# Performance work log

Hardware: AMD Instinct MI355X
Metric: run time of the kernel (lower is better)

Reference implementation:

```python
import jax, jax.numpy as jnp
import numpy as np

B, S, D, H, E, K = 4, 2048, 1024, 4096, 8, 2


def setup_inputs() -> dict:
    key = jax.random.key(0)
    ks = jax.random.split(key, 8)
    scale = 0.02
    x = jax.random.normal(ks[0], (B, S, D), dtype=jnp.float32)
    gate_w = jax.random.normal(ks[1], (D, E), dtype=jnp.float32) * scale
    gate_b = jnp.zeros((E,), dtype=jnp.float32)
    w1 = jax.random.normal(ks[2], (E, D, H), dtype=jnp.float32) * scale
    b1 = jnp.zeros((E, H), dtype=jnp.float32)
    w2 = jax.random.normal(ks[3], (E, H, D), dtype=jnp.float32) * scale
    b2 = jnp.zeros((E, D), dtype=jnp.float32)
    return {"x": x, "gate_w": gate_w, "gate_b": gate_b,
            "w1": w1, "b1": b1, "w2": w2, "b2": b2}


def reference(x, gate_w, gate_b, w1, b1, w2, b2):
    b, s, d = x.shape
    xf = x.reshape(-1, d)                              # [T, D]
    T = xf.shape[0]
    gates = xf @ gate_w + gate_b                       # [T, E]
    scores, idx = jax.lax.top_k(gates, K)              # [T, K] each
    g = jax.nn.softmax(scores, axis=-1)                # softmax over top-k slots
    # Per-token, per-expert combine weight (top-k indices are distinct)
    Wte = jnp.zeros((T, E), dtype=xf.dtype).at[jnp.arange(T)[:, None], idx].add(g)
    # Loop over the small fixed expert set via scan, accumulating weighted outputs.
    def body(acc, p):
        w1e, b1e, w2e, b2e, we = p                     # we: [T]
        h = jax.nn.gelu(xf @ w1e + b1e, approximate=False)  # [T, H]
        y = h @ w2e + b2e                              # [T, D]
        return acc + we[:, None] * y, None
    out, _ = jax.lax.scan(body, jnp.zeros_like(xf), (w1, b1, w2, b2, Wte.T))
    return out.reshape(b, s, d)
```

## Files before the change

kernel.cpp:

```cpp
#include <hip/hip_runtime.h>
#include <hip/hip_bf16.h>

#define Bb 4
#define Ss 2048
#define Dd 1024
#define Hh 4096
#define Ee 8
#define Tt (Bb*Ss)

typedef __attribute__((ext_vector_type(8))) short short8;
typedef __attribute__((ext_vector_type(4))) float floatx4;
typedef unsigned short u16;
typedef unsigned int u32;

__device__ __forceinline__ u16 f2bf(float f) {
  union { float f; u32 u; } v; v.f = f;
  return (u16)((v.u + 0x7FFFu + ((v.u >> 16) & 1u)) >> 16);
}

__global__ __launch_bounds__(256) void cvt_x(const float* __restrict__ x, u16* __restrict__ xb) {
  size_t i = ((size_t)blockIdx.x * 256 + threadIdx.x) * 8;
  float4 a = *(const float4*)(x + i);
  float4 b = *(const float4*)(x + i + 4);
  union { u16 us[8]; uint4 v; } o;
  o.us[0] = f2bf(a.x); o.us[1] = f2bf(a.y); o.us[2] = f2bf(a.z); o.us[3] = f2bf(a.w);
  o.us[4] = f2bf(b.x); o.us[5] = f2bf(b.y); o.us[6] = f2bf(b.z); o.us[7] = f2bf(b.w);
  *(uint4*)(xb + i) = o.v;
}

__global__ __launch_bounds__(256) void tconv(const float* __restrict__ src, u16* __restrict__ dst,
                                             int R, int C) {
  __shared__ float tile[64][65];
  int e = blockIdx.z;
  int r0 = blockIdx.y * 64, c0 = blockIdx.x * 64;
  int tx = threadIdx.x & 63, ty = threadIdx.x >> 6;
  const float* s = src + (size_t)e * R * C;
  u16* d = dst + (size_t)e * R * C;
#pragma unroll
  for (int i = 0; i < 16; i++) {
    int r = i * 4 + ty;
    tile[r][tx] = s[(size_t)(r0 + r) * C + c0 + tx];
  }
  __syncthreads();
#pragma unroll
  for (int i = 0; i < 16; i++) {
    int c = i * 4 + ty;
    d[(size_t)(c0 + c) * R + r0 + tx] = f2bf(tile[tx][c]);
  }
}

__global__ __launch_bounds__(256) void gate_kernel(const float* __restrict__ x,
                                                   const float* __restrict__ gw,
                                                   const float* __restrict__ gb,
                                                   int* __restrict__ counts,
                                                   int* __restrict__ tokL,
                                                   int* __restrict__ pairL,
                                                   float* __restrict__ wtL) {
  __shared__ float gwl[Dd * Ee];
  for (int i = threadIdx.x; i < Dd * Ee; i += 256) gwl[i] = gw[i];
  __syncthreads();
  int wid = threadIdx.x >> 6, lane = threadIdx.x & 63;
  int t = blockIdx.x * 4 + wid;
  const float* xr = x + (size_t)t * Dd;
  double acc[Ee];
#pragma unroll
  for (int e = 0; e < Ee; e++) acc[e] = 0.0;
  for (int i = 0; i < Dd / 64; i++) {
    int d = lane + i * 64;
    float xv = xr[d];
#pragma unroll
    for (int e = 0; e < Ee; e++) acc[e] += (double)xv * (double)gwl[d * Ee + e];
  }
#pragma unroll
  for (int off = 32; off > 0; off >>= 1)
#pragma unroll
    for (int e = 0; e < Ee; e++) acc[e] += __shfl_down(acc[e], off);
  if (lane == 0) {
    float s[Ee];
#pragma unroll
    for (int e = 0; e < Ee; e++) s[e] = (float)acc[e] + gb[e];
    int i0 = 0;
#pragma unroll
    for (int e = 1; e < Ee; e++) if (s[e] > s[i0]) i0 = e;
    int i1 = (i0 == 0) ? 1 : 0;
#pragma unroll
    for (int e = 0; e < Ee; e++) if (e != i0 && s[e] > s[i1]) i1 = e;
    float ex = expf(s[i1] - s[i0]);
    float g0 = 1.0f / (1.0f + ex);
    float g1 = ex / (1.0f + ex);
    int p0 = atomicAdd(&counts[i0], 1);
    tokL[i0 * Tt + p0] = t; pairL[i0 * Tt + p0] = t * 2;     wtL[i0 * Tt + p0] = g0;
    int p1 = atomicAdd(&counts[i1], 1);
    tokL[i1 * Tt + p1] = t; pairL[i1 * Tt + p1] = t * 2 + 1; wtL[i1 * Tt + p1] = g1;
  }
}

__global__ __launch_bounds__(256) void gemm1(const u16* __restrict__ xb,
                                             const u16* __restrict__ w1t,
                                             const float* __restrict__ b1,
                                             const int* __restrict__ counts,
                                             const int* __restrict__ tokL,
                                             const int* __restrict__ pairL,
                                             u16* __restrict__ h) {
  int e = blockIdx.z;
  int cnt = counts[e];
  int m0 = blockIdx.y * 128;
  if (m0 >= cnt) return;
  int rows = cnt - m0; if (rows > 128) rows = 128;
  int n0 = blockIdx.x * 128;

  __shared__ __align__(16) u16 As[128 * 40];
  __shared__ __align__(16) u16 Bs[128 * 40];
  __shared__ int ltok[128];
  __shared__ int lpair[128];

  int tid = threadIdx.x;
  if (tid < 128) {
    int ok = tid < rows;
    ltok[tid]  = ok ? tokL[e * Tt + m0 + tid] : 0;
    lpair[tid] = ok ? pairL[e * Tt + m0 + tid] : 0;
  }
  __syncthreads();

  floatx4 zero4 = {0.f, 0.f, 0.f, 0.f};
  floatx4 acc[4][4];
#pragma unroll
  for (int i = 0; i < 4; i++)
#pragma unroll
    for (int j = 0; j < 4; j++) acc[i][j] = zero4;

  int wave = tid >> 6, lane = tid & 63;
  int wr = wave >> 1, wc = wave & 1;
  int lm = lane & 15, lq = lane >> 4;

  for (int k0 = 0; k0 < Dd; k0 += 32) {
#pragma unroll
    for (int c = tid; c < 512; c += 256) {
      int row = c >> 2, q = c & 3;
      uint4 av = make_uint4(0, 0, 0, 0);
      if (row < rows) av = *(const uint4*)(xb + (size_t)ltok[row] * Dd + k0 + q * 8);
      *(uint4*)(As + row * 40 + q * 8) = av;
      *(uint4*)(Bs + row * 40 + q * 8) =
          *(const uint4*)(w1t + ((size_t)e * Hh + n0 + row) * Dd + k0 + q * 8);
    }
    __syncthreads();
    short8 a[4], b[4];
#pragma unroll
    for (int i = 0; i < 4; i++) a[i] = *(const short8*)(As + (wr * 64 + i * 16 + lm) * 40 + lq * 8);
#pragma unroll
    for (int j = 0; j < 4; j++) b[j] = *(const short8*)(Bs + (wc * 64 + j * 16 + lm) * 40 + lq * 8);
#pragma unroll
    for (int i = 0; i < 4; i++)
#pragma unroll
      for (int j = 0; j < 4; j++)
        acc[i][j] = __builtin_amdgcn_mfma_f32_16x16x32_bf16(a[i], b[j], acc[i][j], 0, 0, 0);
    __syncthreads();
  }

#pragma unroll
  for (int i = 0; i < 4; i++) {
    int rbase = wr * 64 + i * 16 + lq * 4;
#pragma unroll
    for (int r = 0; r < 4; r++) {
      int row = rbase + r;
      if (row < rows) {
        int p = lpair[row];
#pragma unroll
        for (int j = 0; j < 4; j++) {
          int col = n0 + wc * 64 + j * 16 + lm;
          float v = acc[i][j][r] + b1[e * Hh + col];
          v = 0.5f * v * (1.0f + erff(v * 0.70710678118f));
          h[(size_t)p * Hh + col] = f2bf(v);
        }
      }
    }
  }
}

__global__ __launch_bounds__(256) void gemm2(const u16* __restrict__ h,
                                             const u16* __restrict__ w2t,
                                             const float* __restrict__ b2,
                                             const int* __restrict__ counts,
                                             const int* __restrict__ tokL,
                                             const int* __restrict__ pairL,
                                             const float* __restrict__ wtL,
                                             float* __restrict__ out) {
  int e = blockIdx.z;
  int cnt = counts[e];
  int m0 = blockIdx.y * 128;
  if (m0 >= cnt) return;
  int rows = cnt - m0; if (rows > 128) rows = 128;
  int n0 = blockIdx.x * 128;

  __shared__ __align__(16) u16 As[128 * 40];
  __shared__ __align__(16) u16 Bs[128 * 40];
  __shared__ int ltok[128];
  __shared__ int lpair[128];
  __shared__ float lwt[128];

  int tid = threadIdx.x;
  if (tid < 128) {
    int ok = tid < rows;
    ltok[tid]  = ok ? tokL[e * Tt + m0 + tid] : 0;
    lpair[tid] = ok ? pairL[e * Tt + m0 + tid] : 0;
    lwt[tid]   = ok ? wtL[e * Tt + m0 + tid] : 0.f;
  }
  __syncthreads();

  floatx4 zero4 = {0.f, 0.f, 0.f, 0.f};
  floatx4 acc[4][4];
#pragma unroll
  for (int i = 0; i < 4; i++)
#pragma unroll
    for (int j = 0; j < 4; j++) acc[i][j] = zero4;

  int wave = tid >> 6, lane = tid & 63;
  int wr = wave >> 1, wc = wave & 1;
  int lm = lane & 15, lq = lane >> 4;

  for (int k0 = 0; k0 < Hh; k0 += 32) {
#pragma unroll
    for (int c = tid; c < 512; c += 256) {
      int row = c >> 2, q = c & 3;
      uint4 av = make_uint4(0, 0, 0, 0);
      if (row < rows) av = *(const uint4*)(h + (size_t)lpair[row] * Hh + k0 + q * 8);
      *(uint4*)(As + row * 40 + q * 8) = av;
      *(uint4*)(Bs + row * 40 + q * 8) =
          *(const uint4*)(w2t + ((size_t)e * Dd + n0 + row) * Hh + k0 + q * 8);
    }
    __syncthreads();
    short8 a[4], b[4];
#pragma unroll
    for (int i = 0; i < 4; i++) a[i] = *(const short8*)(As + (wr * 64 + i * 16 + lm) * 40 + lq * 8);
#pragma unroll
    for (int j = 0; j < 4; j++) b[j] = *(const short8*)(Bs + (wc * 64 + j * 16 + lm) * 40 + lq * 8);
#pragma unroll
    for (int i = 0; i < 4; i++)
#pragma unroll
      for (int j = 0; j < 4; j++)
        acc[i][j] = __builtin_amdgcn_mfma_f32_16x16x32_bf16(a[i], b[j], acc[i][j], 0, 0, 0);
    __syncthreads();
  }

#pragma unroll
  for (int i = 0; i < 4; i++) {
    int rbase = wr * 64 + i * 16 + lq * 4;
#pragma unroll
    for (int r = 0; r < 4; r++) {
      int row = rbase + r;
      if (row < rows) {
        int t = ltok[row];
        float w = lwt[row];
#pragma unroll
        for (int j = 0; j < 4; j++) {
          int col = n0 + wc * 64 + j * 16 + lm;
          float v = (acc[i][j][r] + b2[e * Dd + col]) * w;
          atomicAdd(out + (size_t)t * Dd + col, v);
        }
      }
    }
  }
}

extern "C" void kernel_launch(void* const* d_in, const int* in_sizes, int n_in,
                              void* d_out, int out_size, void* d_ws, size_t ws_size,
                              hipStream_t stream) {
  const float* x      = (const float*)d_in[0];
  const float* gate_w = (const float*)d_in[1];
  const float* gate_b = (const float*)d_in[2];
  const float* w1     = (const float*)d_in[3];
  const float* b1     = (const float*)d_in[4];
  const float* w2     = (const float*)d_in[5];
  const float* b2     = (const float*)d_in[6];
  float* out = (float*)d_out;

  char* ws = (char*)d_ws;
  size_t off = 0;
  int* counts = (int*)(ws + off); off += 256;
  int* tokL   = (int*)(ws + off); off += (size_t)Ee * Tt * 4;
  int* pairL  = (int*)(ws + off); off += (size_t)Ee * Tt * 4;
  float* wtL  = (float*)(ws + off); off += (size_t)Ee * Tt * 4;
  u16* xb     = (u16*)(ws + off); off += (size_t)Tt * Dd * 2;
  u16* w1t    = (u16*)(ws + off); off += (size_t)Ee * Hh * Dd * 2;
  u16* w2t    = (u16*)(ws + off); off += (size_t)Ee * Dd * Hh * 2;
  u16* hbuf   = (u16*)(ws + off); off += (size_t)Tt * 2 * Hh * 2;

  hipMemsetAsync(counts, 0, 256, stream);
  hipMemsetAsync(out, 0, (size_t)Tt * Dd * 4, stream);

  cvt_x<<<(Tt * Dd) / (256 * 8), 256, 0, stream>>>(x, xb);
  tconv<<<dim3(Hh / 64, Dd / 64, Ee), 256, 0, stream>>>(w1, w1t, Dd, Hh);
  tconv<<<dim3(Dd / 64, Hh / 64, Ee), 256, 0, stream>>>(w2, w2t, Hh, Dd);
  gate_kernel<<<Tt / 4, 256, 0, stream>>>(x, gate_w, gate_b, counts, tokL, pairL, wtL);
  gemm1<<<dim3(Hh / 128, Tt / 128, Ee), 256, 0, stream>>>(xb, w1t, b1, counts, tokL, pairL, hbuf);
  gemm2<<<dim3(Dd / 128, Tt / 128, Ee), 256, 0, stream>>>(hbuf, w2t, b2, counts, tokL, pairL, wtL, out);
}
```

Before: 1.278 ms.

## Use direct global-to-LDS loads with XOR swizzle and grouped tile ordering in expert GEMMs

```diff
diff --git a/kernel.cpp b/kernel.cpp
--- a/kernel.cpp
+++ b/kernel.cpp
@@ -16,6 +16,12 @@
 __device__ __forceinline__ u16 f2bf(float f) {
   union { float f; u32 u; } v; v.f = f;
   return (u16)((v.u + 0x7FFFu + ((v.u >> 16) & 1u)) >> 16);
+}
+
+__device__ __forceinline__ void async16(const u16* g, u16* l) {
+  __builtin_amdgcn_global_load_lds(
+      (const __attribute__((address_space(1))) unsigned int*)g,
+      (__attribute__((address_space(3))) unsigned int*)l, 16, 0, 0);
 }
 
 __global__ __launch_bounds__(256) void cvt_x(const float* __restrict__ x, u16* __restrict__ xb) {
@@ -102,58 +108,87 @@
                                              const int* __restrict__ tokL,
                                              const int* __restrict__ pairL,
                                              u16* __restrict__ h) {
+  const int NT = 32;
   int e = blockIdx.z;
   int cnt = counts[e];
-  int m0 = blockIdx.y * 128;
+  int flat = blockIdx.x + NT * blockIdx.y;
+  int x8 = flat & 7, j = flat >> 3;
+  int n_t = j % NT;
+  int m_t = (j / NT) * 8 + x8;
+  int m0 = m_t * 128;
   if (m0 >= cnt) return;
   int rows = cnt - m0; if (rows > 128) rows = 128;
-  int n0 = blockIdx.x * 128;
-
-  __shared__ __align__(16) u16 As[128 * 40];
-  __shared__ __align__(16) u16 Bs[128 * 40];
+  int n0 = n_t * 128;
+
+  __shared__ __align__(16) u16 As[128 * 32];
+  __shared__ __align__(16) u16 Bs[128 * 32];
   __shared__ int ltok[128];
   __shared__ int lpair[128];
 
   int tid = threadIdx.x;
   if (tid < 128) {
     int ok = tid < rows;
-    ltok[tid]  = ok ? tokL[e * Tt + m0 + tid] : 0;
+    ltok[tid]  = ok ? tokL[e * Tt + m0 + tid] : tokL[e * Tt + m0];
     lpair[tid] = ok ? pairL[e * Tt + m0 + tid] : 0;
   }
   __syncthreads();
+
+  int wv = tid >> 6, ln = tid & 63;
+  int half = wv & 1;
+  const u16* gp[4];
+  u16* ldst[4];
+  if (wv < 2) {
+#pragma unroll
+    for (int q = 0; q < 4; q++) {
+      int r = half * 64 + q * 16 + (ln >> 2);
+      int c = (ln & 3) ^ ((r >> 1) & 3);
+      gp[q] = xb + (size_t)ltok[r] * Dd + c * 8;
+      ldst[q] = As + (half * 64 + q * 16) * 32;
+    }
+  } else {
+#pragma unroll
+    for (int q = 0; q < 4; q++) {
+      int r = half * 64 + q * 16 + (ln >> 2);
+      int c = (ln & 3) ^ ((r >> 1) & 3);
+      gp[q] = w1t + ((size_t)e * Hh + n0 + r) * Dd + c * 8;
+      ldst[q] = Bs + (half * 64 + q * 16) * 32;
+    }
+  }
 
   floatx4 zero4 = {0.f, 0.f, 0.f, 0.f};
   floatx4 acc[4][4];
 #pragma unroll
   for (int i = 0; i < 4; i++)
 #pragma unroll
-    for (int j = 0; j < 4; j++) acc[i][j] = zero4;
-
-  int wave = tid >> 6, lane = tid & 63;
-  int wr = wave >> 1, wc = wave & 1;
-  int lm = lane & 15, lq = lane >> 4;
+    for (int jj = 0; jj < 4; jj++) acc[i][jj] = zero4;
+
+  int wr = wv >> 1, wc = wv & 1;
+  int lm = ln & 15, lq = ln >> 4;
 
   for (int k0 = 0; k0 < Dd; k0 += 32) {
 #pragma unroll
-    for (int c = tid; c < 512; c += 256) {
-      int row = c >> 2, q = c & 3;
-      uint4 av = make_uint4(0, 0, 0, 0);
-      if (row < rows) av = *(const uint4*)(xb + (size_t)ltok[row] * Dd + k0 + q * 8);
-      *(uint4*)(As + row * 40 + q * 8) = av;
-      *(uint4*)(Bs + row * 40 + q * 8) =
-          *(const uint4*)(w1t + ((size_t)e * Hh + n0 + row) * Dd + k0 + q * 8);
-    }
+    for (int q = 0; q < 4; q++) async16(gp[q], ldst[q]);
+#pragma unroll
+    for (int q = 0; q < 4; q++) gp[q] += 32;
     __syncthreads();
     short8 a[4], b[4];
 #pragma unroll
-    for (int i = 0; i < 4; i++) a[i] = *(const short8*)(As + (wr * 64 + i * 16 + lm) * 40 + lq * 8);
-#pragma unroll
-    for (int j = 0; j < 4; j++) b[j] = *(const short8*)(Bs + (wc * 64 + j * 16 + lm) * 40 + lq * 8);
+    for (int i = 0; i < 4; i++) {
+      int row = wr * 64 + i * 16 + lm;
+      int p = lq ^ ((row >> 1) & 3);
+      a[i] = *(const short8*)(As + row * 32 + p * 8);
+    }
+#pragma unroll
+    for (int jj = 0; jj < 4; jj++) {
+      int row = wc * 64 + jj * 16 + lm;
+      int p = lq ^ ((row >> 1) & 3);
+      b[jj] = *(const short8*)(Bs + row * 32 + p * 8);
+    }
 #pragma unroll
     for (int i = 0; i < 4; i++)
 #pragma unroll
-      for (int j = 0; j < 4; j++)
-        acc[i][j] = __builtin_amdgcn_mfma_f32_16x16x32_bf16(a[i], b[j], acc[i][j], 0, 0, 0);
+      for (int jj = 0; jj < 4; jj++)
+        acc[i][jj] = __builtin_amdgcn_mfma_f32_16x16x32_bf16(a[i], b[jj], acc[i][jj], 0, 0, 0);
     __syncthreads();
   }
 
@@ -166,9 +201,9 @@
       if (row < rows) {
         int p = lpair[row];
 #pragma unroll
-        for (int j = 0; j < 4; j++) {
-          int col = n0 + wc * 64 + j * 16 + lm;
-          float v = acc[i][j][r] + b1[e * Hh + col];
+        for (int jj = 0; jj < 4; jj++) {
+          int col = n0 + wc * 64 + jj * 16 + lm;
+          float v = acc[i][jj][r] + b1[e * Hh + col];
           v = 0.5f * v * (1.0f + erff(v * 0.70710678118f));
           h[(size_t)p * Hh + col] = f2bf(v);
         }
@@ -185,15 +220,20 @@
                                              const int* __restrict__ pairL,
                                              const float* __restrict__ wtL,
                                              float* __restrict__ out) {
+  const int NT = 8;
   int e = blockIdx.z;
   int cnt = counts[e];
-  int m0 = blockIdx.y * 128;
+  int flat = blockIdx.x + NT * blockIdx.y;
+  int x8 = flat & 7, j = flat >> 3;
+  int n_t = j % NT;
+  int m_t = (j / NT) * 8 + x8;
+  int m0 = m_t * 128;
   if (m0 >= cnt) return;
   int rows = cnt - m0; if (rows > 128) rows = 128;
-  int n0 = blockIdx.x * 128;
-
-  __shared__ __align__(16) u16 As[128 * 40];
-  __shared__ __align__(16) u16 Bs[128 * 40];
+  int n0 = n_t * 128;
+
+  __shared__ __align__(16) u16 As[128 * 32];
+  __shared__ __align__(16) u16 Bs[128 * 32];
   __shared__ int ltok[128];
   __shared__ int lpair[128];
   __shared__ float lwt[128];
@@ -202,43 +242,67 @@
   if (tid < 128) {
     int ok = tid < rows;
     ltok[tid]  = ok ? tokL[e * Tt + m0 + tid] : 0;
-    lpair[tid] = ok ? pairL[e * Tt + m0 + tid] : 0;
+    lpair[tid] = ok ? pairL[e * Tt + m0 + tid] : pairL[e * Tt + m0];
     lwt[tid]   = ok ? wtL[e * Tt + m0 + tid] : 0.f;
   }
   __syncthreads();
+
+  int wv = tid >> 6, ln = tid & 63;
+  int half = wv & 1;
+  const u16* gp[4];
+  u16* ldst[4];
+  if (wv < 2) {
+#pragma unroll
+    for (int q = 0; q < 4; q++) {
+      int r = half * 64 + q * 16 + (ln >> 2);
+      int c = (ln & 3) ^ ((r >> 1) & 3);
+      gp[q] = h + (size_t)lpair[r] * Hh + c * 8;
+      ldst[q] = As + (half * 64 + q * 16) * 32;
+    }
+  } else {
+#pragma unroll
+    for (int q = 0; q < 4; q++) {
+      int r = half * 64 + q * 16 + (ln >> 2);
+      int c = (ln & 3) ^ ((r >> 1) & 3);
+      gp[q] = w2t + ((size_t)e * Dd + n0 + r) * Hh + c * 8;
+      ldst[q] = Bs + (half * 64 + q * 16) * 32;
+    }
+  }
 
   floatx4 zero4 = {0.f, 0.f, 0.f, 0.f};
   floatx4 acc[4][4];
 #pragma unroll
   for (int i = 0; i < 4; i++)
 #pragma unroll
-    for (int j = 0; j < 4; j++) acc[i][j] = zero4;
-
-  int wave = tid >> 6, lane = tid & 63;
-  int wr = wave >> 1, wc = wave & 1;
-  int lm = lane & 15, lq = lane >> 4;
+    for (int jj = 0; jj < 4; jj++) acc[i][jj] = zero4;
+
+  int wr = wv >> 1, wc = wv & 1;
+  int lm = ln & 15, lq = ln >> 4;
 
   for (int k0 = 0; k0 < Hh; k0 += 32) {
 #pragma unroll
-    for (int c = tid; c < 512; c += 256) {
-      int row = c >> 2, q = c & 3;
-      uint4 av = make_uint4(0, 0, 0, 0);
-      if (row < rows) av = *(const uint4*)(h + (size_t)lpair[row] * Hh + k0 + q * 8);
-      *(uint4*)(As + row * 40 + q * 8) = av;
-      *(uint4*)(Bs + row * 40 + q * 8) =
-          *(const uint4*)(w2t + ((size_t)e * Dd + n0 + row) * Hh + k0 + q * 8);
-    }
+    for (int q = 0; q < 4; q++) async16(gp[q], ldst[q]);
+#pragma unroll
+    for (int q = 0; q < 4; q++) gp[q] += 32;
     __syncthreads();
     short8 a[4], b[4];
 #pragma unroll
-    for (int i = 0; i < 4; i++) a[i] = *(const short8*)(As + (wr * 64 + i * 16 + lm) * 40 + lq * 8);
-#pragma unroll
-    for (int j = 0; j < 4; j++) b[j] = *(const short8*)(Bs + (wc * 64 + j * 16 + lm) * 40 + lq * 8);
+    for (int i = 0; i < 4; i++) {
+      int row = wr * 64 + i * 16 + lm;
+      int p = lq ^ ((row >> 1) & 3);
+      a[i] = *(const short8*)(As + row * 32 + p * 8);
+    }
+#pragma unroll
+    for (int jj = 0; jj < 4; jj++) {
+      int row = wc * 64 + jj * 16 + lm;
+      int p = lq ^ ((row >> 1) & 3);
+      b[jj] = *(const short8*)(Bs + row * 32 + p * 8);
+    }
 #pragma unroll
     for (int i = 0; i < 4; i++)
 #pragma unroll
-      for (int j = 0; j < 4; j++)
-        acc[i][j] = __builtin_amdgcn_mfma_f32_16x16x32_bf16(a[i], b[j], acc[i][j], 0, 0, 0);
+      for (int jj = 0; jj < 4; jj++)
+        acc[i][jj] = __builtin_amdgcn_mfma_f32_16x16x32_bf16(a[i], b[jj], acc[i][jj], 0, 0, 0);
     __syncthreads();
   }
 
@@ -252,9 +316,9 @@
         int t = ltok[row];
         float w = lwt[row];
 #pragma unroll
-        for (int j = 0; j < 4; j++) {
-          int col = n0 + wc * 64 + j * 16 + lm;
-          float v = (acc[i][j][r] + b2[e * Dd + col]) * w;
+        for (int jj = 0; jj < 4; jj++) {
+          int col = n0 + wc * 64 + jj * 16 + lm;
+          float v = (acc[i][jj][r] + b2[e * Dd + col]) * w;
           atomicAdd(out + (size_t)t * Dd + col, v);
         }
       }
@@ -292,6 +356,6 @@
   tconv<<<dim3(Hh / 64, Dd / 64, Ee), 256, 0, stream>>>(w1, w1t, Dd, Hh);
   tconv<<<dim3(Dd / 64, Hh / 64, Ee), 256, 0, stream>>>(w2, w2t, Hh, Dd);
   gate_kernel<<<Tt / 4, 256, 0, stream>>>(x, gate_w, gate_b, counts, tokL, pairL, wtL);
-  gemm1<<<dim3(Hh / 128, Tt / 128, Ee), 256, 0, stream>>>(xb, w1t, b1, counts, tokL, pairL, hbuf);
-  gemm2<<<dim3(Dd / 128, Tt / 128, Ee), 256, 0, stream>>>(hbuf, w2t, b2, counts, tokL, pairL, wtL, out);
-}
+  gemm1<<<dim3(32, 64, Ee), 256, 0, stream>>>(xb, w1t, b1, counts, tokL, pairL, hbuf);
+  gemm2<<<dim3(8, 64, Ee), 256, 0, stream>>>(hbuf, w2t, b2, counts, tokL, pairL, wtL, out);
+}
```

New measurement: 1.120 ms. 1.14x faster.
